# Kernel tuning notes

Hardware: AMD Instinct MI355X
Metric: run time of the kernel (lower is better)

The kernel has to match this reference:

```python
import jax, jax.numpy as jnp
import numpy as np

N, Fdim, Aout = 8192, 32, 8
AVG_DEG = 32.0  # target average degree for the random graph


def setup_inputs() -> dict:
    key = jax.random.key(0)
    ks = jax.random.split(key, 12)
    x = jax.random.normal(ks[0], (N, Fdim), dtype=jnp.float32)
    # binary adjacency, zero diagonal (GCNConv adds self-loops itself)
    u = jax.random.uniform(ks[1], (N, N), dtype=jnp.float32)
    adj = (u < (AVG_DEG / N)).astype(jnp.float32)
    adj = adj * (1.0 - jnp.eye(N, dtype=jnp.float32))
    mask = (jax.random.uniform(ks[2], (N,), dtype=jnp.float32) < 0.5).astype(jnp.float32)

    def lin(k, fout, fin):
        s = 1.0 / np.sqrt(fin)
        return jax.random.uniform(k, (fout, fin), jnp.float32, -s, s)

    return {
        "x": x, "adj": adj, "mask": mask,
        "w1": lin(ks[3], 64, Fdim), "b1": jnp.zeros((64,), jnp.float32),
        "w2": lin(ks[4], 128, 64), "b2": jnp.zeros((128,), jnp.float32),
        "wg": lin(ks[5], 128, 128), "bg": jnp.zeros((128,), jnp.float32),
        "wd": lin(ks[6], 128, 128), "bd": jnp.zeros((128,), jnp.float32),
        "wp1": lin(ks[7], 128, 256), "bp1": jnp.zeros((128,), jnp.float32),
        "wp2": lin(ks[8], 64, 128), "bp2": jnp.zeros((64,), jnp.float32),
        "wo": lin(ks[9], Aout, 64), "bo": jnp.zeros((Aout,), jnp.float32),
    }


def reference(x, adj, mask, w1, b1, w2, b2, wg, bg, wd, bd, wp1, bp1, wp2, bp2, wo, bo):
    # encoder MLP
    h = jax.nn.relu(x @ w1.T + b1)           # [N,64]
    h = jax.nn.relu(h @ w2.T + b2)           # [N,128]
    # GCNConv with default self-loops and symmetric normalization:
    # out = D^{-1/2} (A + I) D^{-1/2} (h W^T) + b
    a_hat = adj + jnp.eye(adj.shape[0], dtype=adj.dtype)
    deg = jnp.sum(a_hat, axis=1)             # >= 1 thanks to self-loops
    dinv = jax.lax.rsqrt(deg)
    msg = h @ wg.T                            # [N,128]
    agg = dinv[:, None] * (a_hat @ (dinv[:, None] * msg))  # normalized aggregation
    g = jax.nn.relu(agg + bg)
    g = jax.nn.relu(g @ wd.T + bd)
    f = jnp.concatenate([g, h], axis=1)       # [N,256]
    p = jax.nn.relu(f @ wp1.T + bp1)
    p = jax.nn.relu(p @ wp2.T + bp2)
    out = (p @ wo.T + bo) * mask[:, None]     # [N,Aout]
    return out
```

## Files before the change

kernel.cpp:

```cpp
#include <hip/hip_runtime.h>

#define N_NODES 8192
#define CAP 128

__global__ void deg_csr_kernel(const float* __restrict__ adj,
                               int* __restrict__ cnt, int* __restrict__ nbr,
                               float* __restrict__ dinv) {
  __shared__ int s_cnt;
  const int row = blockIdx.x;
  const int t = threadIdx.x;
  if (t == 0) s_cnt = 0;
  __syncthreads();
  const float4* rowp = (const float4*)(adj + (size_t)row * N_NODES);
#pragma unroll
  for (int i = 0; i < 8; ++i) {
    int idx4 = t + i * 256;
    float4 v = rowp[idx4];
    int col = idx4 * 4;
    if (v.x != 0.f) { int p = atomicAdd(&s_cnt, 1); if (p < CAP) nbr[row * CAP + p] = col; }
    if (v.y != 0.f) { int p = atomicAdd(&s_cnt, 1); if (p < CAP) nbr[row * CAP + p] = col + 1; }
    if (v.z != 0.f) { int p = atomicAdd(&s_cnt, 1); if (p < CAP) nbr[row * CAP + p] = col + 2; }
    if (v.w != 0.f) { int p = atomicAdd(&s_cnt, 1); if (p < CAP) nbr[row * CAP + p] = col + 3; }
  }
  __syncthreads();
  if (t == 0) {
    cnt[row] = s_cnt;
    dinv[row] = rsqrtf((float)s_cnt + 1.0f);
  }
}

__global__ void agg_kernel(const int* __restrict__ cnt, const int* __restrict__ nbr,
                           const float* __restrict__ msg, const float* __restrict__ dinv,
                           const float* __restrict__ bg, const float* __restrict__ adj,
                           float* __restrict__ g1) {
  const int row = blockIdx.x;
  const int t = threadIdx.x;
  float acc = msg[(size_t)row * 128 + t];
  const int c = cnt[row];
  if (c <= CAP) {
    for (int i = 0; i < c; ++i) {
      int j = nbr[row * CAP + i];
      acc += msg[(size_t)j * 128 + t];
    }
  } else {
    for (int col = 0; col < N_NODES; ++col) {
      if (adj[(size_t)row * N_NODES + col] != 0.f) acc += msg[(size_t)col * 128 + t];
    }
  }
  float v = fmaf(dinv[row], acc, bg[t]);
  g1[(size_t)row * 128 + t] = fmaxf(v, 0.f);
}

template <int K, int FOUT, int MODE, bool CONCAT>
__launch_bounds__(256)
__global__ void gemm_kernel(const float* __restrict__ A, const float* __restrict__ A2,
                            const float* __restrict__ W, const float* __restrict__ bias,
                            const float* __restrict__ rowscale, float* __restrict__ C) {
  constexpr int ROWS = 32, KC = 32;
  constexpr int NCH = K / KC;
  constexpr int RSTRIDE = 256 / FOUT;
  constexpr int RPT = ROWS / RSTRIDE;
  __shared__ float A_lds[ROWS][KC + 4];
  __shared__ float W_lds[KC][FOUT + 1];
  const int t = threadIdx.x;
  const int n0 = blockIdx.x * ROWS;
  const int c = t % FOUT;
  const int rbase = t / FOUT;
  float acc[RPT];
#pragma unroll
  for (int i = 0; i < RPT; ++i) acc[i] = 0.f;

  for (int ch = 0; ch < NCH; ++ch) {
    {
      int row = t >> 3, k4 = (t & 7) * 4;
      int kk = ch * KC + k4;
      const float* src;
      if (CONCAT) {
        src = (kk < K / 2) ? (A + (size_t)(n0 + row) * (K / 2) + kk)
                           : (A2 + (size_t)(n0 + row) * (K / 2) + (kk - K / 2));
      } else {
        src = A + (size_t)(n0 + row) * K + kk;
      }
      float4 v = *(const float4*)src;
      *(float4*)&A_lds[row][k4] = v;
    }
#pragma unroll
    for (int i = 0; i < (FOUT * KC) / 256; ++i) {
      int lin = t + i * 256;
      int k = lin & (KC - 1), f = lin >> 5;
      W_lds[k][f] = W[(size_t)f * K + ch * KC + k];
    }
    __syncthreads();
#pragma unroll
    for (int kg = 0; kg < KC / 4; ++kg) {
      float w0 = W_lds[kg * 4 + 0][c];
      float w1v = W_lds[kg * 4 + 1][c];
      float w2v = W_lds[kg * 4 + 2][c];
      float w3v = W_lds[kg * 4 + 3][c];
#pragma unroll
      for (int i = 0; i < RPT; ++i) {
        const float4 av = *(const float4*)&A_lds[rbase + i * RSTRIDE][kg * 4];
        acc[i] = fmaf(av.x, w0, acc[i]);
        acc[i] = fmaf(av.y, w1v, acc[i]);
        acc[i] = fmaf(av.z, w2v, acc[i]);
        acc[i] = fmaf(av.w, w3v, acc[i]);
      }
    }
    __syncthreads();
  }
#pragma unroll
  for (int i = 0; i < RPT; ++i) {
    int node = n0 + rbase + i * RSTRIDE;
    float v = acc[i];
    if (MODE & 1) v += bias[c];
    if (MODE & 2) v = fmaxf(v, 0.f);
    if (MODE & 4) v *= rowscale[node];
    C[(size_t)node * FOUT + c] = v;
  }
}

extern "C" void kernel_launch(void* const* d_in, const int* in_sizes, int n_in,
                              void* d_out, int out_size, void* d_ws, size_t ws_size,
                              hipStream_t stream) {
  const float* x    = (const float*)d_in[0];
  const float* adj  = (const float*)d_in[1];
  const float* mask = (const float*)d_in[2];
  const float* w1   = (const float*)d_in[3];
  const float* b1   = (const float*)d_in[4];
  const float* w2   = (const float*)d_in[5];
  const float* b2   = (const float*)d_in[6];
  const float* wg   = (const float*)d_in[7];
  const float* bg   = (const float*)d_in[8];
  const float* wd   = (const float*)d_in[9];
  const float* bd   = (const float*)d_in[10];
  const float* wp1  = (const float*)d_in[11];
  const float* bp1  = (const float*)d_in[12];
  const float* wp2  = (const float*)d_in[13];
  const float* bp2  = (const float*)d_in[14];
  const float* wo   = (const float*)d_in[15];
  const float* bo   = (const float*)d_in[16];
  float* out = (float*)d_out;

  float* ws = (float*)d_ws;
  float* h1   = ws; ws += (size_t)N_NODES * 64;
  float* h    = ws; ws += (size_t)N_NODES * 128;
  float* msg  = ws; ws += (size_t)N_NODES * 128;
  float* g1   = ws; ws += (size_t)N_NODES * 128;
  float* g2   = ws; ws += (size_t)N_NODES * 128;
  float* p1   = ws; ws += (size_t)N_NODES * 128;
  float* p2   = ws; ws += (size_t)N_NODES * 64;
  float* dinv = ws; ws += N_NODES;
  int* cnt = (int*)ws; ws += N_NODES;
  int* nbr = (int*)ws;

  deg_csr_kernel<<<N_NODES, 256, 0, stream>>>(adj, cnt, nbr, dinv);
  gemm_kernel<32, 64, 3, false><<<256, 256, 0, stream>>>(x, nullptr, w1, b1, nullptr, h1);
  gemm_kernel<64, 128, 3, false><<<256, 256, 0, stream>>>(h1, nullptr, w2, b2, nullptr, h);
  gemm_kernel<128, 128, 4, false><<<256, 256, 0, stream>>>(h, nullptr, wg, nullptr, dinv, msg);
  agg_kernel<<<N_NODES, 128, 0, stream>>>(cnt, nbr, msg, dinv, bg, adj, g1);
  gemm_kernel<128, 128, 3, false><<<256, 256, 0, stream>>>(g1, nullptr, wd, bd, nullptr, g2);
  gemm_kernel<256, 128, 3, true><<<256, 256, 0, stream>>>(g2, h, wp1, bp1, nullptr, p1);
  gemm_kernel<128, 64, 3, false><<<256, 256, 0, stream>>>(p1, nullptr, wp2, bp2, nullptr, p2);
  gemm_kernel<64, 8, 5, false><<<256, 256, 0, stream>>>(p2, nullptr, wo, bo, mask, out);
}
```

Before: 514.6 us.

## Fuse encoder MLP with adjacency scan, fuse decoder layers, use wave ballot compaction

```diff
diff --git a/kernel.cpp b/kernel.cpp
--- a/kernel.cpp
+++ b/kernel.cpp
@@ -2,121 +2,184 @@
 
 #define N_NODES 8192
 #define CAP 128
-
-__global__ void deg_csr_kernel(const float* __restrict__ adj,
-                               int* __restrict__ cnt, int* __restrict__ nbr,
-                               float* __restrict__ dinv) {
-  __shared__ int s_cnt;
+#define SCAN_BLOCKS 2048
+#define ENC_BLOCKS 256
+#define TILE 32
+constexpr int AST = 132;
+constexpr int WST = 129;
+
+template <int K, int KSPLIT, int F, bool RELU, bool BIAS, bool MASK>
+__device__ __forceinline__ void layer_op(
+    const float (*__restrict__ A0)[AST], const float (*__restrict__ A1)[AST],
+    float (*__restrict__ Aout)[AST], float (*__restrict__ Wb)[WST],
+    const float* __restrict__ W, const float* __restrict__ bias,
+    float* __restrict__ gout, const float* __restrict__ rowmask,
+    int n0, int t) {
+  constexpr int KC = 32;
+  constexpr int NCH = K / KC;
+  constexpr int RS = 256 / F;
+  constexpr int RPT = TILE / RS;
+  const int c = t % F;
+  const int rb = t / F;
+  float acc[RPT];
+#pragma unroll
+  for (int i = 0; i < RPT; ++i) acc[i] = 0.f;
+
+  for (int ch = 0; ch < NCH; ++ch) {
+#pragma unroll
+    for (int i = 0; i < (F * KC + 255) / 256; ++i) {
+      int lin = t + i * 256;
+      if ((F * KC) % 256 == 0 || lin < F * KC) {
+        int k = lin % KC, f = lin / KC;
+        Wb[k][f] = W[(size_t)f * K + ch * KC + k];
+      }
+    }
+    __syncthreads();
+    const float (*__restrict__ As)[AST] = (ch * KC < KSPLIT) ? A0 : A1;
+    const int kb = (ch * KC < KSPLIT) ? ch * KC : ch * KC - KSPLIT;
+#pragma unroll
+    for (int kg = 0; kg < KC / 4; ++kg) {
+      float w0 = Wb[kg * 4 + 0][c];
+      float w1 = Wb[kg * 4 + 1][c];
+      float w2 = Wb[kg * 4 + 2][c];
+      float w3 = Wb[kg * 4 + 3][c];
+#pragma unroll
+      for (int i = 0; i < RPT; ++i) {
+        const float4 a = *(const float4*)&As[rb + i * RS][kb + kg * 4];
+        acc[i] = fmaf(a.x, w0, acc[i]);
+        acc[i] = fmaf(a.y, w1, acc[i]);
+        acc[i] = fmaf(a.z, w2, acc[i]);
+        acc[i] = fmaf(a.w, w3, acc[i]);
+      }
+    }
+    __syncthreads();
+  }
+#pragma unroll
+  for (int i = 0; i < RPT; ++i) {
+    float v = acc[i];
+    if (BIAS) v += bias[c];
+    if (RELU) v = fmaxf(v, 0.f);
+    int node = n0 + rb + i * RS;
+    if (MASK) v *= rowmask[node];
+    if (Aout) Aout[rb + i * RS][c] = v;
+    if (gout) gout[(size_t)node * F + c] = v;
+  }
+}
+
+__global__ __launch_bounds__(256) void scan_encode_kernel(
+    const float* __restrict__ adj, const float* __restrict__ x,
+    const float* __restrict__ w1, const float* __restrict__ b1,
+    const float* __restrict__ w2, const float* __restrict__ b2,
+    const float* __restrict__ wg,
+    int* __restrict__ cnt, int* __restrict__ nbr, float* __restrict__ dinv,
+    float* __restrict__ h_out, float* __restrict__ msg_out) {
+  __shared__ float bufA[TILE][AST];
+  __shared__ float bufB[TILE][AST];
+  __shared__ float Wb[32][WST];
+  const int t = threadIdx.x;
+
+  if (blockIdx.x < SCAN_BLOCKS) {
+    const int lane = t & 63;
+    const int row = blockIdx.x * 4 + (t >> 6);
+    const float4* rowp = (const float4*)(adj + (size_t)row * N_NODES);
+    const unsigned long long lmask = (1ull << lane) - 1;
+    int off = 0;
+    for (int it = 0; it < N_NODES / 4 / 64; ++it) {
+      const int idx4 = lane + it * 64;
+      const float4 v = rowp[idx4];
+      const int col = idx4 * 4;
+      {
+        unsigned long long m = __ballot(v.x != 0.f);
+        if (m) { if (v.x != 0.f) { int p = off + __popcll(m & lmask); if (p < CAP) nbr[row * CAP + p] = col; } off += __popcll(m); }
+      }
+      {
+        unsigned long long m = __ballot(v.y != 0.f);
+        if (m) { if (v.y != 0.f) { int p = off + __popcll(m & lmask); if (p < CAP) nbr[row * CAP + p] = col + 1; } off += __popcll(m); }
+      }
+      {
+        unsigned long long m = __ballot(v.z != 0.f);
+        if (m) { if (v.z != 0.f) { int p = off + __popcll(m & lmask); if (p < CAP) nbr[row * CAP + p] = col + 2; } off += __popcll(m); }
+      }
+      {
+        unsigned long long m = __ballot(v.w != 0.f);
+        if (m) { if (v.w != 0.f) { int p = off + __popcll(m & lmask); if (p < CAP) nbr[row * CAP + p] = col + 3; } off += __popcll(m); }
+      }
+    }
+    if (lane == 0) {
+      cnt[row] = off;
+      dinv[row] = rsqrtf((float)off + 1.0f);
+    }
+  } else {
+    const int n0 = (blockIdx.x - SCAN_BLOCKS) * TILE;
+    {
+      int row = t >> 3, k4 = (t & 7) * 4;
+      *(float4*)&bufA[row][k4] = *(const float4*)&x[(size_t)(n0 + row) * 32 + k4];
+    }
+    layer_op<32, 32, 64, true, true, false>(bufA, nullptr, bufB, Wb, w1, b1, nullptr, nullptr, n0, t);
+    layer_op<64, 64, 128, true, true, false>(bufB, nullptr, bufA, Wb, w2, b2, h_out, nullptr, n0, t);
+    layer_op<128, 128, 128, false, false, false>(bufA, nullptr, nullptr, Wb, wg, nullptr, msg_out, nullptr, n0, t);
+  }
+}
+
+__global__ __launch_bounds__(128) void agg_kernel(
+    const int* __restrict__ cnt, const int* __restrict__ nbr,
+    const float* __restrict__ msg, const float* __restrict__ dinv,
+    const float* __restrict__ bg, const float* __restrict__ adj,
+    float* __restrict__ g1) {
   const int row = blockIdx.x;
   const int t = threadIdx.x;
-  if (t == 0) s_cnt = 0;
-  __syncthreads();
-  const float4* rowp = (const float4*)(adj + (size_t)row * N_NODES);
-#pragma unroll
-  for (int i = 0; i < 8; ++i) {
-    int idx4 = t + i * 256;
-    float4 v = rowp[idx4];
-    int col = idx4 * 4;
-    if (v.x != 0.f) { int p = atomicAdd(&s_cnt, 1); if (p < CAP) nbr[row * CAP + p] = col; }
-    if (v.y != 0.f) { int p = atomicAdd(&s_cnt, 1); if (p < CAP) nbr[row * CAP + p] = col + 1; }
-    if (v.z != 0.f) { int p = atomicAdd(&s_cnt, 1); if (p < CAP) nbr[row * CAP + p] = col + 2; }
-    if (v.w != 0.f) { int p = atomicAdd(&s_cnt, 1); if (p < CAP) nbr[row * CAP + p] = col + 3; }
-  }
-  __syncthreads();
-  if (t == 0) {
-    cnt[row] = s_cnt;
-    dinv[row] = rsqrtf((float)s_cnt + 1.0f);
-  }
-}
-
-__global__ void agg_kernel(const int* __restrict__ cnt, const int* __restrict__ nbr,
-                           const float* __restrict__ msg, const float* __restrict__ dinv,
-                           const float* __restrict__ bg, const float* __restrict__ adj,
-                           float* __restrict__ g1) {
-  const int row = blockIdx.x;
-  const int t = threadIdx.x;
-  float acc = msg[(size_t)row * 128 + t];
+  float acc = dinv[row] * msg[(size_t)row * 128 + t];
   const int c = cnt[row];
   if (c <= CAP) {
-    for (int i = 0; i < c; ++i) {
+    int i = 0;
+    for (; i + 4 <= c; i += 4) {
+      int j0 = nbr[row * CAP + i + 0];
+      int j1 = nbr[row * CAP + i + 1];
+      int j2 = nbr[row * CAP + i + 2];
+      int j3 = nbr[row * CAP + i + 3];
+      float a0 = dinv[j0] * msg[(size_t)j0 * 128 + t];
+      float a1 = dinv[j1] * msg[(size_t)j1 * 128 + t];
+      float a2 = dinv[j2] * msg[(size_t)j2 * 128 + t];
+      float a3 = dinv[j3] * msg[(size_t)j3 * 128 + t];
+      acc += (a0 + a1) + (a2 + a3);
+    }
+    for (; i < c; ++i) {
       int j = nbr[row * CAP + i];
-      acc += msg[(size_t)j * 128 + t];
+      acc += dinv[j] * msg[(size_t)j * 128 + t];
     }
   } else {
     for (int col = 0; col < N_NODES; ++col) {
-      if (adj[(size_t)row * N_NODES + col] != 0.f) acc += msg[(size_t)col * 128 + t];
+      if (adj[(size_t)row * N_NODES + col] != 0.f) acc += dinv[col] * msg[(size_t)col * 128 + t];
     }
   }
   float v = fmaf(dinv[row], acc, bg[t]);
   g1[(size_t)row * 128 + t] = fmaxf(v, 0.f);
 }
 
-template <int K, int FOUT, int MODE, bool CONCAT>
-__launch_bounds__(256)
-__global__ void gemm_kernel(const float* __restrict__ A, const float* __restrict__ A2,
-                            const float* __restrict__ W, const float* __restrict__ bias,
-                            const float* __restrict__ rowscale, float* __restrict__ C) {
-  constexpr int ROWS = 32, KC = 32;
-  constexpr int NCH = K / KC;
-  constexpr int RSTRIDE = 256 / FOUT;
-  constexpr int RPT = ROWS / RSTRIDE;
-  __shared__ float A_lds[ROWS][KC + 4];
-  __shared__ float W_lds[KC][FOUT + 1];
+__global__ __launch_bounds__(256) void decode_kernel(
+    const float* __restrict__ g1, const float* __restrict__ h,
+    const float* __restrict__ wd, const float* __restrict__ bd,
+    const float* __restrict__ wp1, const float* __restrict__ bp1,
+    const float* __restrict__ wp2, const float* __restrict__ bp2,
+    const float* __restrict__ wo, const float* __restrict__ bo,
+    const float* __restrict__ mask, float* __restrict__ out) {
+  __shared__ float bufA[TILE][AST];
+  __shared__ float bufB[TILE][AST];
+  __shared__ float bufH[TILE][AST];
+  __shared__ float Wb[32][WST];
   const int t = threadIdx.x;
-  const int n0 = blockIdx.x * ROWS;
-  const int c = t % FOUT;
-  const int rbase = t / FOUT;
-  float acc[RPT];
-#pragma unroll
-  for (int i = 0; i < RPT; ++i) acc[i] = 0.f;
-
-  for (int ch = 0; ch < NCH; ++ch) {
-    {
-      int row = t >> 3, k4 = (t & 7) * 4;
-      int kk = ch * KC + k4;
-      const float* src;
-      if (CONCAT) {
-        src = (kk < K / 2) ? (A + (size_t)(n0 + row) * (K / 2) + kk)
-                           : (A2 + (size_t)(n0 + row) * (K / 2) + (kk - K / 2));
-      } else {
-        src = A + (size_t)(n0 + row) * K + kk;
-      }
-      float4 v = *(const float4*)src;
-      *(float4*)&A_lds[row][k4] = v;
-    }
-#pragma unroll
-    for (int i = 0; i < (FOUT * KC) / 256; ++i) {
-      int lin = t + i * 256;
-      int k = lin & (KC - 1), f = lin >> 5;
-      W_lds[k][f] = W[(size_t)f * K + ch * KC + k];
-    }
-    __syncthreads();
-#pragma unroll
-    for (int kg = 0; kg < KC / 4; ++kg) {
-      float w0 = W_lds[kg * 4 + 0][c];
-      float w1v = W_lds[kg * 4 + 1][c];
-      float w2v = W_lds[kg * 4 + 2][c];
-      float w3v = W_lds[kg * 4 + 3][c];
-#pragma unroll
-      for (int i = 0; i < RPT; ++i) {
-        const float4 av = *(const float4*)&A_lds[rbase + i * RSTRIDE][kg * 4];
-        acc[i] = fmaf(av.x, w0, acc[i]);
-        acc[i] = fmaf(av.y, w1v, acc[i]);
-        acc[i] = fmaf(av.z, w2v, acc[i]);
-        acc[i] = fmaf(av.w, w3v, acc[i]);
-      }
-    }
-    __syncthreads();
-  }
-#pragma unroll
-  for (int i = 0; i < RPT; ++i) {
-    int node = n0 + rbase + i * RSTRIDE;
-    float v = acc[i];
-    if (MODE & 1) v += bias[c];
-    if (MODE & 2) v = fmaxf(v, 0.f);
-    if (MODE & 4) v *= rowscale[node];
-    C[(size_t)node * FOUT + c] = v;
-  }
+  const int n0 = blockIdx.x * TILE;
+#pragma unroll
+  for (int i = 0; i < 4; ++i) {
+    int lin = t + i * 256;
+    int row = lin >> 5, k4 = (lin & 31) * 4;
+    *(float4*)&bufA[row][k4] = *(const float4*)&g1[(size_t)(n0 + row) * 128 + k4];
+    *(float4*)&bufH[row][k4] = *(const float4*)&h[(size_t)(n0 + row) * 128 + k4];
+  }
+  layer_op<128, 128, 128, true, true, false>(bufA, nullptr, bufB, Wb, wd, bd, nullptr, nullptr, n0, t);
+  layer_op<256, 128, 128, true, true, false>(bufB, bufH, bufA, Wb, wp1, bp1, nullptr, nullptr, n0, t);
+  layer_op<128, 128, 64, true, true, false>(bufA, nullptr, bufB, Wb, wp2, bp2, nullptr, nullptr, n0, t);
+  layer_op<64, 64, 8, false, true, true>(bufB, nullptr, nullptr, Wb, wo, bo, out, mask, n0, t);
 }
 
 extern "C" void kernel_launch(void* const* d_in, const int* in_sizes, int n_in,
@@ -142,24 +205,16 @@
   float* out = (float*)d_out;
 
   float* ws = (float*)d_ws;
-  float* h1   = ws; ws += (size_t)N_NODES * 64;
   float* h    = ws; ws += (size_t)N_NODES * 128;
   float* msg  = ws; ws += (size_t)N_NODES * 128;
   float* g1   = ws; ws += (size_t)N_NODES * 128;
-  float* g2   = ws; ws += (size_t)N_NODES * 128;
-  float* p1   = ws; ws += (size_t)N_NODES * 128;
-  float* p2   = ws; ws += (size_t)N_NODES * 64;
   float* dinv = ws; ws += N_NODES;
   int* cnt = (int*)ws; ws += N_NODES;
   int* nbr = (int*)ws;
 
-  deg_csr_kernel<<<N_NODES, 256, 0, stream>>>(adj, cnt, nbr, dinv);
-  gemm_kernel<32, 64, 3, false><<<256, 256, 0, stream>>>(x, nullptr, w1, b1, nullptr, h1);
-  gemm_kernel<64, 128, 3, false><<<256, 256, 0, stream>>>(h1, nullptr, w2, b2, nullptr, h);
-  gemm_kernel<128, 128, 4, false><<<256, 256, 0, stream>>>(h, nullptr, wg, nullptr, dinv, msg);
+  scan_encode_kernel<<<SCAN_BLOCKS + ENC_BLOCKS, 256, 0, stream>>>(
+      adj, x, w1, b1, w2, b2, wg, cnt, nbr, dinv, h, msg);
   agg_kernel<<<N_NODES, 128, 0, stream>>>(cnt, nbr, msg, dinv, bg, adj, g1);
-  gemm_kernel<128, 128, 3, false><<<256, 256, 0, stream>>>(g1, nullptr, wd, bd, nullptr, g2);
-  gemm_kernel<256, 128, 3, true><<<256, 256, 0, stream>>>(g2, h, wp1, bp1, nullptr, p1);
-  gemm_kernel<128, 64, 3, false><<<256, 256, 0, stream>>>(p1, nullptr, wp2, bp2, nullptr, p2);
-  gemm_kernel<64, 8, 5, false><<<256, 256, 0, stream>>>(p2, nullptr, wo, bo, mask, out);
-}
+  decode_kernel<<<N_NODES / TILE, 256, 0, stream>>>(
+      g1, h, wd, bd, wp1, bp1, wp2, bp2, wo, bo, mask, out);
+}
```

New measurement: 673.7 us. 30.9% more time.
